# Kernel optimization log

Hardware: AMD Instinct MI355X
Metric: run time of the kernel (lower is better)

The kernel has to match this reference:

```python
import jax, jax.numpy as jnp
import numpy as np

N_NODES = 100000
N_EDGES = 1600000
NIN = 128
NOUT = 128


def setup_inputs() -> dict:
    key = jax.random.key(0)
    k1, k2, k3, k4, k5 = jax.random.split(key, 5)
    x = jax.random.normal(k1, (N_NODES, NIN), dtype=jnp.float32)
    edge_index = jax.random.randint(k2, (2, N_EDGES), 0, N_NODES, dtype=jnp.int32)
    edge_attr = jax.random.uniform(k3, (N_EDGES,), dtype=jnp.float32)
    # GCNConv linear weight (glorot-ish scale) and bias
    W = jax.random.normal(k4, (NIN, NOUT), dtype=jnp.float32) / np.sqrt(NIN)
    b = jnp.zeros((NOUT,), dtype=jnp.float32)
    return {"x": x, "edge_index": edge_index, "edge_attr": edge_attr, "W": W, "b": b}


def reference(x, edge_index, edge_attr, W, b):
    # PyG GCNConv: out = D^{-1/2} (A + I) D^{-1/2} X W + b
    # edge_attr is accepted by the wrapper's forward but ignored.
    N = x.shape[0]
    src, dst = edge_index[0], edge_index[1]
    # add self-loops
    loops = jnp.arange(N, dtype=edge_index.dtype)
    src = jnp.concatenate([src, loops])
    dst = jnp.concatenate([dst, loops])
    # degree over destination nodes (unit edge weights + self loops)
    deg = jax.ops.segment_sum(jnp.ones_like(dst, dtype=x.dtype), dst, num_segments=N)
    dinv = jnp.where(deg > 0, jax.lax.rsqrt(deg), 0.0)
    norm = dinv[src] * dinv[dst]  # [E + N]
    h = x @ W  # [N, NOUT] — project before aggregation (PyG order)
    msgs = h[src] * norm[:, None]  # [E + N, NOUT] gathered messages
    out = jax.ops.segment_sum(msgs, dst, num_segments=N) + b
    return out
```

## Files before the change

### kernel.cpp

```cpp
#include <hip/hip_runtime.h>
#include <hip/hip_bf16.h>


#define NIN 128
#define NOUT 128
#define NPART 8
#define SCAT_B 256
#define MAXD 64
#define WT_PITCH 136

typedef __attribute__((ext_vector_type(8))) short short8;
typedef __attribute__((ext_vector_type(4))) float f32x4;
typedef __attribute__((ext_vector_type(4))) int   i32x4;
typedef __attribute__((ext_vector_type(4))) float f32x4v;

__device__ __forceinline__ float bf2f(unsigned short u) {
    unsigned v = ((unsigned)u) << 16;
    return __uint_as_float(v);
}
__device__ __forceinline__ unsigned short f2bf(float f) {
    unsigned u = __float_as_uint(f);
    unsigned r = 0x7FFFu + ((u >> 16) & 1u);
    return (unsigned short)((u + r) >> 16);
}

__global__ __launch_bounds__(256) void k_build(const float* __restrict__ x,
                                               const float* __restrict__ W,
                                               const int* __restrict__ ei,
                                               int* __restrict__ cnt,
                                               int* __restrict__ adj,
                                               unsigned short* __restrict__ h,
                                               int E, int N, int gb) {
    __shared__ unsigned short Wt[128 * WT_PITCH];

    int grp   = blockIdx.x >> 4;
    int lane8 = blockIdx.x & 7;
    int rid   = grp * 8 + lane8;

    if ((blockIdx.x >> 3) & 1) {
        int p = lane8;
        int c = grp;
        int PS = (N + NPART - 1) / NPART;
        int lo = p * PS, hi = min(N, lo + PS);
        int chunkE = (((E + SCAT_B - 1) / SCAT_B) + 3) & ~3;
        int e0 = c * chunkE, e1 = min(E, e0 + chunkE);
        for (int e = e0 + (int)threadIdx.x * 4; e < e1; e += 1024) {
            i32x4 s4 = __builtin_nontemporal_load((const i32x4*)(ei + e));
            i32x4 d4 = __builtin_nontemporal_load((const i32x4*)(ei + E + e));
            #pragma unroll
            for (int k = 0; k < 4; k++) {
                int d = d4[k];
                if (d >= lo && d < hi) {
                    int pos = atomicAdd(&cnt[d], 1);
                    if (pos < MAXD) adj[(size_t)d * MAXD + pos] = s4[k];
                }
            }
        }
        return;
    }

    if (rid >= gb) return;

    for (int idx = threadIdx.x; idx < NIN * NOUT; idx += 256) {
        int k = idx >> 7, n = idx & 127;
        Wt[n * WT_PITCH + k] = f2bf(W[idx]);
    }
    __syncthreads();

    int wave = threadIdx.x >> 6, lane = threadIdx.x & 63;
    int node_base = rid * 64 + wave * 16;
    if (node_base >= N) return;

    int c = lane & 15, quad = lane >> 4;

    short8 a[4];
    const f32x4v* xrow = (const f32x4v*)(x + (size_t)(node_base + c) * NIN + quad * 8);
    #pragma unroll
    for (int kt = 0; kt < 4; kt++) {
        f32x4v f0 = __builtin_nontemporal_load(xrow + kt * 8);
        f32x4v f1 = __builtin_nontemporal_load(xrow + kt * 8 + 1);
        short8 af;
        af[0] = (short)f2bf(f0[0]); af[1] = (short)f2bf(f0[1]);
        af[2] = (short)f2bf(f0[2]); af[3] = (short)f2bf(f0[3]);
        af[4] = (short)f2bf(f1[0]); af[5] = (short)f2bf(f1[1]);
        af[6] = (short)f2bf(f1[2]); af[7] = (short)f2bf(f1[3]);
        a[kt] = af;
    }

    f32x4 acc[8];
    #pragma unroll
    for (int nt = 0; nt < 8; nt++) acc[nt] = (f32x4)(0.0f);

    #pragma unroll
    for (int nt = 0; nt < 8; nt++) {
        const unsigned short* wp = &Wt[(nt * 16 + c) * WT_PITCH + quad * 8];
        #pragma unroll
        for (int kt = 0; kt < 4; kt++) {
            short8 bfrag = *(const short8*)(wp + kt * 32);
            acc[nt] = __builtin_amdgcn_mfma_f32_16x16x32_bf16(a[kt], bfrag, acc[nt], 0, 0, 0);
        }
    }

    #pragma unroll
    for (int nt = 0; nt < 8; nt++) {
        #pragma unroll
        for (int r = 0; r < 4; r++) {
            int node = node_base + quad * 4 + r;
            h[(size_t)node * NOUT + nt * 16 + c] = f2bf(acc[nt][r]);
        }
    }
}

__global__ __launch_bounds__(256) void k_agg(const unsigned short* __restrict__ h,
                                             const int* __restrict__ cnt,
                                             const int* __restrict__ adj,
                                             const float* __restrict__ bias,
                                             float* __restrict__ out, int N) {
    int wave = threadIdx.x >> 6, lane = threadIdx.x & 63;
    int half = lane >> 5, sub = lane & 31;
    int node = blockIdx.x * 4 + wave;
    if (node >= N) return;

    int degc = cnt[node];
    float dn = rsqrtf((float)(degc + 1));
    int e0 = node * MAXD;
    int e1 = e0 + min(degc, MAXD);

    const uint2* hp = (const uint2*)h;
    float a0 = 0.f, a1 = 0.f, a2 = 0.f, a3 = 0.f;

    {
        int s = node; float ds = dn;
        if (half) {
            if (e0 < e1) { s = adj[e0]; ds = rsqrtf((float)(cnt[s] + 1)); }
            else ds = 0.f;
        }
        uint2 v = hp[(size_t)s * 32 + sub];
        a0 += bf2f((unsigned short)(v.x & 0xFFFF)) * ds;
        a1 += bf2f((unsigned short)(v.x >> 16)) * ds;
        a2 += bf2f((unsigned short)(v.y & 0xFFFF)) * ds;
        a3 += bf2f((unsigned short)(v.y >> 16)) * ds;
    }

    int e = e0 + 1;
    for (; e + 7 < e1; e += 8) {
        #pragma unroll
        for (int k = 0; k < 4; k++) {
            int s = adj[e + 2 * k + half];
            float ds = rsqrtf((float)(cnt[s] + 1));
            uint2 v = hp[(size_t)s * 32 + sub];
            a0 += bf2f((unsigned short)(v.x & 0xFFFF)) * ds;
            a1 += bf2f((unsigned short)(v.x >> 16)) * ds;
            a2 += bf2f((unsigned short)(v.y & 0xFFFF)) * ds;
            a3 += bf2f((unsigned short)(v.y >> 16)) * ds;
        }
    }
    for (; e + 1 < e1; e += 2) {
        int s = adj[e + half];
        float ds = rsqrtf((float)(cnt[s] + 1));
        uint2 v = hp[(size_t)s * 32 + sub];
        a0 += bf2f((unsigned short)(v.x & 0xFFFF)) * ds;
        a1 += bf2f((unsigned short)(v.x >> 16)) * ds;
        a2 += bf2f((unsigned short)(v.y & 0xFFFF)) * ds;
        a3 += bf2f((unsigned short)(v.y >> 16)) * ds;
    }
    if (e < e1) {
        int s = adj[e];
        uint2 v = hp[(size_t)s * 32 + sub];
        if (!half) {
            float ds = rsqrtf((float)(cnt[s] + 1));
            a0 += bf2f((unsigned short)(v.x & 0xFFFF)) * ds;
            a1 += bf2f((unsigned short)(v.x >> 16)) * ds;
            a2 += bf2f((unsigned short)(v.y & 0xFFFF)) * ds;
            a3 += bf2f((unsigned short)(v.y >> 16)) * ds;
        }
    }

    a0 += __shfl_xor(a0, 32);
    a1 += __shfl_xor(a1, 32);
    a2 += __shfl_xor(a2, 32);
    a3 += __shfl_xor(a3, 32);

    if (!half) {
        float4 b4 = ((const float4*)bias)[sub];
        f32x4 o;
        o[0] = a0 * dn + b4.x;
        o[1] = a1 * dn + b4.y;
        o[2] = a2 * dn + b4.z;
        o[3] = a3 * dn + b4.w;
        __builtin_nontemporal_store(o, (f32x4*)(out + (size_t)node * NOUT) + sub);
    }
}

static inline size_t align256(size_t v) { return (v + 255) & ~(size_t)255; }

extern "C" void kernel_launch(void* const* d_in, const int* in_sizes, int n_in,
                              void* d_out, int out_size, void* d_ws, size_t ws_size,
                              hipStream_t stream) {
    const float* x  = (const float*)d_in[0];
    const int*   ei = (const int*)d_in[1];
    const float* W  = (const float*)d_in[3];
    const float* b  = (const float*)d_in[4];
    float*       out = (float*)d_out;

    int N = in_sizes[0] / NIN;
    int E = in_sizes[1] / 2;
    int gb = (N + 63) / 64;

    char* ws = (char*)d_ws;
    size_t o = 0;
    int*   cnt = (int*)(ws + o);   o += align256((size_t)N * 4);
    int*   adj = (int*)(ws + o);   o += align256((size_t)N * MAXD * 4);
    unsigned short* h = (unsigned short*)(ws + o); o += align256((size_t)N * NOUT * 2);
    (void)ws_size; (void)n_in; (void)out_size;

    hipMemsetAsync(cnt, 0, (size_t)N * 4, stream);
    k_build<<<16 * SCAT_B, 256, 0, stream>>>(x, W, ei, cnt, adj, h, E, N, gb);
    k_agg<<<(N + 3) / 4, 256, 0, stream>>>(h, cnt, adj, b, out, N);
}
```

Measured before the change: 300.3 us.

## Halve LDS weight tile in two K passes and regroup build grid

The GEMM blocks now stage only half of W (64 K-rows, pitch 68) in shared memory at a time and run two passes with extra barriers. This halves LDS use so 8 blocks per CU fit, as set by the launch bound. The grid is regrouped so each group of 32 blocks holds 16 GEMM and 16 scatter blocks, with 196 edge chunks instead of 256. Edge-index loads switch from nontemporal to normal loads. In exchange, the W conversion is done twice per block and more barriers are added.

```diff
diff --git a/kernel.cpp b/kernel.cpp
--- a/kernel.cpp
+++ b/kernel.cpp
@@ -5,9 +5,9 @@
 #define NIN 128
 #define NOUT 128
 #define NPART 8
-#define SCAT_B 256
+#define G_GROUPS 98
 #define MAXD 64
-#define WT_PITCH 136
+#define WPITCH 68
 
 typedef __attribute__((ext_vector_type(8))) short short8;
 typedef __attribute__((ext_vector_type(4))) float f32x4;
@@ -24,29 +24,30 @@
     return (unsigned short)((u + r) >> 16);
 }
 
-__global__ __launch_bounds__(256) void k_build(const float* __restrict__ x,
-                                               const float* __restrict__ W,
-                                               const int* __restrict__ ei,
-                                               int* __restrict__ cnt,
-                                               int* __restrict__ adj,
-                                               unsigned short* __restrict__ h,
-                                               int E, int N, int gb) {
-    __shared__ unsigned short Wt[128 * WT_PITCH];
-
-    int grp   = blockIdx.x >> 4;
-    int lane8 = blockIdx.x & 7;
-    int rid   = grp * 8 + lane8;
-
-    if ((blockIdx.x >> 3) & 1) {
-        int p = lane8;
-        int c = grp;
+__global__ __launch_bounds__(256, 8) void k_build(const float* __restrict__ x,
+                                                  const float* __restrict__ W,
+                                                  const int* __restrict__ ei,
+                                                  int* __restrict__ cnt,
+                                                  int* __restrict__ adj,
+                                                  unsigned short* __restrict__ h,
+                                                  int E, int N, int gb) {
+    __shared__ unsigned short Wt[128 * WPITCH];
+
+    int grp = blockIdx.x >> 5;
+    int s   = blockIdx.x & 31;
+
+    if ((s & 15) >= 8) {
+        int p = s & 7;
+        int o = (s >> 4) & 1;
+        int c = grp * 2 + o;
         int PS = (N + NPART - 1) / NPART;
         int lo = p * PS, hi = min(N, lo + PS);
-        int chunkE = (((E + SCAT_B - 1) / SCAT_B) + 3) & ~3;
+        int nchunk = 2 * G_GROUPS;
+        int chunkE = (((E + nchunk - 1) / nchunk) + 3) & ~3;
         int e0 = c * chunkE, e1 = min(E, e0 + chunkE);
         for (int e = e0 + (int)threadIdx.x * 4; e < e1; e += 1024) {
-            i32x4 s4 = __builtin_nontemporal_load((const i32x4*)(ei + e));
-            i32x4 d4 = __builtin_nontemporal_load((const i32x4*)(ei + E + e));
+            i32x4 s4 = *(const i32x4*)(ei + e);
+            i32x4 d4 = *(const i32x4*)(ei + E + e);
             #pragma unroll
             for (int k = 0; k < 4; k++) {
                 int d = d4[k];
@@ -59,54 +60,83 @@
         return;
     }
 
+    int rid = grp * 16 + (s & 7) + ((s >> 4) & 1) * 8;
     if (rid >= gb) return;
-
-    for (int idx = threadIdx.x; idx < NIN * NOUT; idx += 256) {
-        int k = idx >> 7, n = idx & 127;
-        Wt[n * WT_PITCH + k] = f2bf(W[idx]);
-    }
-    __syncthreads();
 
     int wave = threadIdx.x >> 6, lane = threadIdx.x & 63;
     int node_base = rid * 64 + wave * 16;
-    if (node_base >= N) return;
-
+    bool active = node_base < N;
     int c = lane & 15, quad = lane >> 4;
 
-    short8 a[4];
     const f32x4v* xrow = (const f32x4v*)(x + (size_t)(node_base + c) * NIN + quad * 8);
-    #pragma unroll
-    for (int kt = 0; kt < 4; kt++) {
-        f32x4v f0 = __builtin_nontemporal_load(xrow + kt * 8);
-        f32x4v f1 = __builtin_nontemporal_load(xrow + kt * 8 + 1);
-        short8 af;
-        af[0] = (short)f2bf(f0[0]); af[1] = (short)f2bf(f0[1]);
-        af[2] = (short)f2bf(f0[2]); af[3] = (short)f2bf(f0[3]);
-        af[4] = (short)f2bf(f1[0]); af[5] = (short)f2bf(f1[1]);
-        af[6] = (short)f2bf(f1[2]); af[7] = (short)f2bf(f1[3]);
-        a[kt] = af;
-    }
 
     f32x4 acc[8];
     #pragma unroll
     for (int nt = 0; nt < 8; nt++) acc[nt] = (f32x4)(0.0f);
 
-    #pragma unroll
-    for (int nt = 0; nt < 8; nt++) {
-        const unsigned short* wp = &Wt[(nt * 16 + c) * WT_PITCH + quad * 8];
-        #pragma unroll
-        for (int kt = 0; kt < 4; kt++) {
-            short8 bfrag = *(const short8*)(wp + kt * 32);
-            acc[nt] = __builtin_amdgcn_mfma_f32_16x16x32_bf16(a[kt], bfrag, acc[nt], 0, 0, 0);
-        }
-    }
-
-    #pragma unroll
-    for (int nt = 0; nt < 8; nt++) {
-        #pragma unroll
-        for (int r = 0; r < 4; r++) {
-            int node = node_base + quad * 4 + r;
-            h[(size_t)node * NOUT + nt * 16 + c] = f2bf(acc[nt][r]);
+    for (int idx = threadIdx.x; idx < 64 * 128; idx += 256) {
+        int kk = idx >> 7, n = idx & 127;
+        Wt[n * WPITCH + kk] = f2bf(W[kk * 128 + n]);
+    }
+    __syncthreads();
+
+    if (active) {
+        short8 a0, a1;
+        {
+            f32x4v f0 = __builtin_nontemporal_load(xrow + 0);
+            f32x4v f1 = __builtin_nontemporal_load(xrow + 1);
+            f32x4v g0 = __builtin_nontemporal_load(xrow + 8);
+            f32x4v g1 = __builtin_nontemporal_load(xrow + 9);
+            a0[0]=(short)f2bf(f0[0]); a0[1]=(short)f2bf(f0[1]); a0[2]=(short)f2bf(f0[2]); a0[3]=(short)f2bf(f0[3]);
+            a0[4]=(short)f2bf(f1[0]); a0[5]=(short)f2bf(f1[1]); a0[6]=(short)f2bf(f1[2]); a0[7]=(short)f2bf(f1[3]);
+            a1[0]=(short)f2bf(g0[0]); a1[1]=(short)f2bf(g0[1]); a1[2]=(short)f2bf(g0[2]); a1[3]=(short)f2bf(g0[3]);
+            a1[4]=(short)f2bf(g1[0]); a1[5]=(short)f2bf(g1[1]); a1[6]=(short)f2bf(g1[2]); a1[7]=(short)f2bf(g1[3]);
+        }
+        #pragma unroll
+        for (int nt = 0; nt < 8; nt++) {
+            const unsigned short* wp = &Wt[(nt * 16 + c) * WPITCH + quad * 8];
+            short8 b0 = *(const short8*)(wp);
+            short8 b1 = *(const short8*)(wp + 32);
+            acc[nt] = __builtin_amdgcn_mfma_f32_16x16x32_bf16(a0, b0, acc[nt], 0, 0, 0);
+            acc[nt] = __builtin_amdgcn_mfma_f32_16x16x32_bf16(a1, b1, acc[nt], 0, 0, 0);
+        }
+    }
+    __syncthreads();
+
+    for (int idx = threadIdx.x; idx < 64 * 128; idx += 256) {
+        int kk = idx >> 7, n = idx & 127;
+        Wt[n * WPITCH + kk] = f2bf(W[(kk + 64) * 128 + n]);
+    }
+    __syncthreads();
+
+    if (active) {
+        short8 a2, a3;
+        {
+            f32x4v f0 = __builtin_nontemporal_load(xrow + 16);
+            f32x4v f1 = __builtin_nontemporal_load(xrow + 17);
+            f32x4v g0 = __builtin_nontemporal_load(xrow + 24);
+            f32x4v g1 = __builtin_nontemporal_load(xrow + 25);
+            a2[0]=(short)f2bf(f0[0]); a2[1]=(short)f2bf(f0[1]); a2[2]=(short)f2bf(f0[2]); a2[3]=(short)f2bf(f0[3]);
+            a2[4]=(short)f2bf(f1[0]); a2[5]=(short)f2bf(f1[1]); a2[6]=(short)f2bf(f1[2]); a2[7]=(short)f2bf(f1[3]);
+            a3[0]=(short)f2bf(g0[0]); a3[1]=(short)f2bf(g0[1]); a3[2]=(short)f2bf(g0[2]); a3[3]=(short)f2bf(g0[3]);
+            a3[4]=(short)f2bf(g1[0]); a3[5]=(short)f2bf(g1[1]); a3[6]=(short)f2bf(g1[2]); a3[7]=(short)f2bf(g1[3]);
+        }
+        #pragma unroll
+        for (int nt = 0; nt < 8; nt++) {
+            const unsigned short* wp = &Wt[(nt * 16 + c) * WPITCH + quad * 8];
+            short8 b0 = *(const short8*)(wp);
+            short8 b1 = *(const short8*)(wp + 32);
+            acc[nt] = __builtin_amdgcn_mfma_f32_16x16x32_bf16(a2, b0, acc[nt], 0, 0, 0);
+            acc[nt] = __builtin_amdgcn_mfma_f32_16x16x32_bf16(a3, b1, acc[nt], 0, 0, 0);
+        }
+
+        #pragma unroll
+        for (int nt = 0; nt < 8; nt++) {
+            #pragma unroll
+            for (int r = 0; r < 4; r++) {
+                int node = node_base + quad * 4 + r;
+                h[(size_t)node * NOUT + nt * 16 + c] = f2bf(acc[nt][r]);
+            }
         }
     }
 }
@@ -215,6 +245,6 @@
     (void)ws_size; (void)n_in; (void)out_size;
 
     hipMemsetAsync(cnt, 0, (size_t)N * 4, stream);
-    k_build<<<16 * SCAT_B, 256, 0, stream>>>(x, W, ei, cnt, adj, h, E, N, gb);
+    k_build<<<32 * G_GROUPS, 256, 0, stream>>>(x, W, ei, cnt, adj, h, E, N, gb);
     k_agg<<<(N + 3) / 4, 256, 0, stream>>>(h, cnt, adj, b, out, N);
 }
```

After: 270.0 us. -10.1%, faster.
